# Optimization experiments

Measured on AMD Instinct MI355X. Metric: run time of the kernel, lower is better.

Reference implementation:

```python
import jax, jax.numpy as jnp
import numpy as np


def _fps_one_batch(pts, num_samples):
    """Furthest point sampling for one batch segment.
    pts: [Npb, 3]. Seeds with point 0 (pointops furthestsampling convention).
    Returns int32 indices [num_samples].
    """
    # initial min-distance to the seed point
    dist = jnp.sum((pts - pts[0]) ** 2, axis=-1)  # [Npb]

    def step(dist, _):
        idx = jnp.argmax(dist)                      # furthest remaining point
        d = jnp.sum((pts - pts[idx]) ** 2, axis=-1)  # dist to new sample
        return jnp.minimum(dist, d), idx.astype(jnp.int32)

    _, idxs = jax.lax.scan(step, dist, None, length=num_samples - 1)
    return jnp.concatenate([jnp.zeros((1,), jnp.int32), idxs])


def setup_inputs() -> dict:
    key = jax.random.key(0)
    N, B = 262144, 2
    Npb = N // B
    xyz = jax.random.normal(key, (N, 3), dtype=jnp.float32) * 20.0  # lidar-scale coords
    b = jnp.repeat(jnp.arange(B, dtype=jnp.float32), Npb)[:, None]
    point_bxyz = jnp.concatenate([b, xyz], axis=1)  # [N, 4] (b, x, y, z)
    return {"point_bxyz": point_bxyz, "stride": 32, "batch_size": B}


def reference(point_bxyz, stride, batch_size):
    N = point_bxyz.shape[0]
    Npb = N // batch_size                      # equal-size batch segments
    M = (Npb + stride - 1) // stride           # samples per batch (ceil)
    xyz = point_bxyz[:, 1:4].reshape(batch_size, Npb, 3)

    idx = jax.vmap(lambda p: _fps_one_batch(p, M))(xyz)          # [B, M] local indices
    gidx = idx + (jnp.arange(batch_size, dtype=jnp.int32) * Npb)[:, None]
    new_bxyz = point_bxyz[gidx.reshape(-1)]    # [B*M, 4] sampled points
    return new_bxyz
```

## Files before the change

kernel.cpp:

```cpp
#include <hip/hip_runtime.h>


#define NB    32
#define TPB   256
#define PPT   16
#define NPB   131072
#define MSAMP 4096
#define RING  2
#define KW    8
#define NWAVE 128
#define NQUAD (NWAVE * 16)
#define RB_U32 (NQUAD * 4)
#define NCAND (NWAVE * KW)
#define JCAP  64

typedef unsigned long long u64;
typedef unsigned int u32;
typedef __attribute__((ext_vector_type(4))) u32 u32x4;

__device__ __forceinline__ void st16_sys(u32* p, u32x4 v) {
  asm volatile("global_store_dwordx4 %0, %1, off sc0 sc1"
               :: "v"(p), "v"(v) : "memory");
}
__device__ __forceinline__ void ld16x8_sys(
    const u32* p0, const u32* p1, const u32* p2, const u32* p3,
    const u32* p4, const u32* p5, const u32* p6, const u32* p7,
    u32x4& q0, u32x4& q1, u32x4& q2, u32x4& q3,
    u32x4& q4, u32x4& q5, u32x4& q6, u32x4& q7) {
  asm volatile(
    "global_load_dwordx4 %0, %8, off sc0 sc1\n\t"
    "global_load_dwordx4 %1, %9, off sc0 sc1\n\t"
    "global_load_dwordx4 %2, %10, off sc0 sc1\n\t"
    "global_load_dwordx4 %3, %11, off sc0 sc1\n\t"
    "global_load_dwordx4 %4, %12, off sc0 sc1\n\t"
    "global_load_dwordx4 %5, %13, off sc0 sc1\n\t"
    "global_load_dwordx4 %6, %14, off sc0 sc1\n\t"
    "global_load_dwordx4 %7, %15, off sc0 sc1\n\t"
    "s_waitcnt vmcnt(0)"
    : "=v"(q0), "=v"(q1), "=v"(q2), "=v"(q3),
      "=v"(q4), "=v"(q5), "=v"(q6), "=v"(q7)
    : "v"(p0), "v"(p1), "v"(p2), "v"(p3),
      "v"(p4), "v"(p5), "v"(p6), "v"(p7)
    : "memory");
}

template<int CTRL>
__device__ __forceinline__ u64 dpp_move64(u64 x) {
  int lo = (int)(u32)(x & 0xFFFFFFFFull);
  int hi = (int)(u32)(x >> 32);
  int nlo = __builtin_amdgcn_update_dpp(lo, lo, CTRL, 0xF, 0xF, false);
  int nhi = __builtin_amdgcn_update_dpp(hi, hi, CTRL, 0xF, 0xF, false);
  return ((u64)(u32)nhi << 32) | (u64)(u32)nlo;
}
#define DPP_ROW_SHR(n)  (0x110 + (n))
#define DPP_BCAST15     0x142
#define DPP_BCAST31     0x143

__device__ __forceinline__ u64 dpp_max64_to63(u64 k) {
  u64 t;
  t = dpp_move64<DPP_ROW_SHR(1)>(k); if (t > k) k = t;
  t = dpp_move64<DPP_ROW_SHR(2)>(k); if (t > k) k = t;
  t = dpp_move64<DPP_ROW_SHR(4)>(k); if (t > k) k = t;
  t = dpp_move64<DPP_ROW_SHR(8)>(k); if (t > k) k = t;
  t = dpp_move64<DPP_BCAST15>(k);    if (t > k) k = t;
  t = dpp_move64<DPP_BCAST31>(k);    if (t > k) k = t;
  return k;
}
__device__ __forceinline__ u64 bcast_key(u64 k, int srclane) {
  u32 lo = (u32)__builtin_amdgcn_readlane((int)(u32)(k & 0xFFFFFFFFull), srclane);
  u32 hi = (u32)__builtin_amdgcn_readlane((int)(u32)(k >> 32), srclane);
  return ((u64)hi << 32) | (u64)lo;
}
__device__ __forceinline__ float bcast_f32(float v, int srclane) {
  return __uint_as_float((u32)__builtin_amdgcn_readlane((int)__float_as_uint(v), srclane));
}

struct BMax { u64 k; float x, y, z; };
__device__ __forceinline__ BMax block_max(u64 tk, float tx, float ty, float tz,
    int lane, int wv, int sb,
    u64* s_key, float* s_cx, float* s_cy, float* s_cz) {
  u64 wk = bcast_key(dpp_max64_to63(tk), 63);
  int wl = __ffsll(__ballot(tk == wk)) - 1;
  float wx = bcast_f32(tx, wl), wy = bcast_f32(ty, wl), wz = bcast_f32(tz, wl);
  if (lane == 0) { s_key[sb+wv]=wk; s_cx[sb+wv]=wx; s_cy[sb+wv]=wy; s_cz[sb+wv]=wz; }
  __syncthreads();
  u64 k0=s_key[sb],k1=s_key[sb+1],k2=s_key[sb+2],k3=s_key[sb+3];
  int bi=sb; u64 bk=k0;
  if (k1>bk){bk=k1;bi=sb+1;}
  if (k2>bk){bk=k2;bi=sb+2;}
  if (k3>bk){bk=k3;bi=sb+3;}
  BMax r; r.k=bk; r.x=s_cx[bi]; r.y=s_cy[bi]; r.z=s_cz[bi];
  return r;
}

template<int NC>
__device__ __forceinline__ int sim_wave(const u32* s_pool, int m, u32 cutd,
    int jmax, int lane, float& ox, float& oy, float& oz) {
#pragma clang fp contract(off)
  u64 ck[NC]; float cx[NC], cy[NC], cz[NC];
#pragma unroll
  for (int i = 0; i < NC; ++i) {
    int idx = lane + i * 64;
    if (idx < m) {
      const u32* b = s_pool + idx * 5;
      ck[i] = ((u64)b[1] << 32) | (u64)b[0];
      cx[i] = __uint_as_float(b[2]); cy[i] = __uint_as_float(b[3]);
      cz[i] = __uint_as_float(b[4]);
    } else { ck[i] = 0; cx[i] = cy[i] = cz[i] = 0.f; }
  }
  int j = 0;
  for (int t = 0; t < jmax; ++t) {
    u64 tk = ck[0]; float mx = cx[0], my = cy[0], mz = cz[0];
#pragma unroll
    for (int i = 1; i < NC; ++i)
      if (ck[i] > tk) { tk = ck[i]; mx = cx[i]; my = cy[i]; mz = cz[i]; }
    u64 wk = bcast_key(dpp_max64_to63(tk), 63);
    if (t > 0 && (u32)(wk >> 32) <= cutd) break;
    int wl = __ffsll(__ballot(tk == wk)) - 1;
    float wx = bcast_f32(mx, wl), wy = bcast_f32(my, wl), wz = bcast_f32(mz, wl);
    if (lane == t) { ox = wx; oy = wy; oz = wz; }
    j = t + 1;
#pragma unroll
    for (int i = 0; i < NC; ++i) {
      float dx = cx[i]-wx, dy = cy[i]-wy, dz = cz[i]-wz;
      float d2 = __fadd_rn(__fadd_rn(__fmul_rn(dx,dx), __fmul_rn(dy,dy)),
                           __fmul_rn(dz,dz));
      float nd = fminf(__uint_as_float((u32)(ck[i] >> 32)), d2);
      ck[i] = ((u64)__float_as_uint(nd) << 32) | (ck[i] & 0xFFFFFFFFull);
    }
  }
  return j;
}

__device__ __forceinline__ int sim_block(const u32* s_pool, int m, u32 cutd,
    int jmax, int tid, int lane, int wv, int& sb,
    u64* s_key, float* s_cx, float* s_cy, float* s_cz, float (*s_win)[3]) {
#pragma clang fp contract(off)
  u64 ck[4]; float cx[4], cy[4], cz[4];
#pragma unroll
  for (int i = 0; i < 4; ++i) {
    int idx = tid + i * 256;
    if (idx < m) {
      const u32* b = s_pool + idx * 5;
      ck[i] = ((u64)b[1] << 32) | (u64)b[0];
      cx[i] = __uint_as_float(b[2]); cy[i] = __uint_as_float(b[3]);
      cz[i] = __uint_as_float(b[4]);
    } else { ck[i] = 0; cx[i] = cy[i] = cz[i] = 0.f; }
  }
  int j = 0;
  for (int t = 0; t < jmax; ++t) {
    u64 tk = ck[0]; float mx = cx[0], my = cy[0], mz = cz[0];
#pragma unroll
    for (int i = 1; i < 4; ++i)
      if (ck[i] > tk) { tk = ck[i]; mx = cx[i]; my = cy[i]; mz = cz[i]; }
    BMax w = block_max(tk, mx, my, mz, lane, wv, sb, s_key, s_cx, s_cy, s_cz);
    sb ^= 4;
    if (t > 0 && (u32)(w.k >> 32) <= cutd) break;
    if (tid == 0) { s_win[t][0]=w.x; s_win[t][1]=w.y; s_win[t][2]=w.z; }
    j = t + 1;
#pragma unroll
    for (int i = 0; i < 4; ++i) {
      float dx = cx[i]-w.x, dy = cy[i]-w.y, dz = cz[i]-w.z;
      float d2 = __fadd_rn(__fadd_rn(__fmul_rn(dx,dx), __fmul_rn(dy,dy)),
                           __fmul_rn(dz,dz));
      float nd = fminf(__uint_as_float((u32)(ck[i] >> 32)), d2);
      ck[i] = ((u64)__float_as_uint(nd) << 32) | (ck[i] & 0xFFFFFFFFull);
    }
  }
  __syncthreads();
  return j;
}

__global__ __launch_bounds__(TPB, 1)
void fps_kernel(const float4* __restrict__ pts, float* __restrict__ out,
                u32* __restrict__ slots)
{
#pragma clang fp contract(off)
  const int batch = blockIdx.x >> 5;
  const int rank  = blockIdx.x & (NB - 1);
  const int tid   = threadIdx.x;
  const int lane  = tid & 63;
  const int wv    = tid >> 6;
  const int ws_id = rank * 4 + wv;

  __shared__ u32   s_quads[NWAVE * 68];
  __shared__ u32   s_pool[NCAND * 5];
  __shared__ float s_win[JCAP][3];
  __shared__ u64   s_key[8];
  __shared__ float s_cx[8], s_cy[8], s_cz[8];
  __shared__ int   s_cnt2[2];

  const float4* bpts = pts + (size_t)batch * NPB;
  u32* bslots = slots + (size_t)batch * (RING * RB_U32);
  const int base = rank * (TPB * PPT);

  float px[PPT], py[PPT], pz[PPT], dist[PPT];
  float4 seed = bpts[0];
  const float sx = seed.y, sy = seed.z, sz = seed.w;
#pragma unroll
  for (int k = 0; k < PPT; ++k) {
    float4 p = bpts[base + k * TPB + tid];
    px[k] = p.y; py[k] = p.z; pz[k] = p.w;
    float dx = px[k]-sx, dy = py[k]-sy, dz = pz[k]-sz;
    dist[k] = __fadd_rn(__fadd_rn(__fmul_rn(dx,dx), __fmul_rn(dy,dy)),
                        __fmul_rn(dz,dz));
  }
  if (rank == 0 && tid == 0) {
    float4 o; o.x=(float)batch; o.y=sx; o.z=sy; o.w=sz;
    *(float4*)(out + (size_t)batch * MSAMP * 4) = o;
  }
  if (tid == 0) { s_cnt2[0] = 0; s_cnt2[1] = 0; }
  __syncthreads();

  int S = 0; u32 r = 0; int sb = 0;

  while (S < MSAMP - 1) {
    r += 1;
    const int rem = (MSAMP - 1) - S;
    const int jmax = (rem < JCAP) ? rem : JCAP;

    u32 mask = 0; u64 tk = 0; float tx=0.f, ty=0.f, tz=0.f; int tbk = 0;
#pragma unroll
    for (int k = 0; k < PPT; ++k) {
      u64 kk = ((u64)__float_as_uint(dist[k]) << 32) | ((u64)r << 17) |
               (u64)(0x1FFFF - (base + k * TPB + tid));
      if (kk > tk) { tk = kk; tx = px[k]; ty = py[k]; tz = pz[k]; tbk = k; }
    }
    u32x4 shipq;
    for (int c = 0; c < KW; ++c) {
      u64 wk = bcast_key(dpp_max64_to63(tk), 63);
      int wl = __ffsll(__ballot(tk == wk)) - 1;
      float wx = bcast_f32(tx, wl), wy = bcast_f32(ty, wl), wz = bcast_f32(tz, wl);
      if (lane == 2*c)     { shipq.x=(u32)(wk & 0xFFFFFFFFull); shipq.y=(u32)(wk>>32);
                             shipq.z=__float_as_uint(wx); shipq.w=__float_as_uint(wy); }
      if (lane == 2*c + 1) { shipq.x=r; shipq.y=__float_as_uint(wz);
                             shipq.z=0u; shipq.w=0u; }
      if (tk == wk) {
        mask |= 1u << tbk;
        tk = 0; tx = ty = tz = 0.f; tbk = 0;
#pragma unroll
        for (int k = 0; k < PPT; ++k) {
          if (!((mask >> k) & 1u)) {
            u64 kk = ((u64)__float_as_uint(dist[k]) << 32) | ((u64)r << 17) |
                     (u64)(0x1FFFF - (base + k * TPB + tid));
            if (kk > tk) { tk = kk; tx = px[k]; ty = py[k]; tz = pz[k]; tbk = k; }
          }
        }
      }
    }

    u32* ring = bslots + (size_t)(r & (RING - 1)) * RB_U32;
    if (lane < 16) st16_sys(ring + (ws_id * 16 + lane) * 4, shipq);

    const int gb = wv * 512 + lane;
    const u32 *pp0 = ring + (gb      ) * 4, *pp1 = ring + (gb +  64) * 4,
              *pp2 = ring + (gb + 128) * 4, *pp3 = ring + (gb + 192) * 4,
              *pp4 = ring + (gb + 256) * 4, *pp5 = ring + (gb + 320) * 4,
              *pp6 = ring + (gb + 384) * 4, *pp7 = ring + (gb + 448) * 4;
    u32x4 q0,q1,q2,q3,q4,q5,q6,q7;
    for (u32 it = 0; ; ++it) {
      ld16x8_sys(pp0,pp1,pp2,pp3,pp4,pp5,pp6,pp7, q0,q1,q2,q3,q4,q5,q6,q7);
      bool ok;
      if ((lane & 1) == 0)
        ok = ((q0.x>>17)==r)&&((q1.x>>17)==r)&&((q2.x>>17)==r)&&((q3.x>>17)==r)&&
             ((q4.x>>17)==r)&&((q5.x>>17)==r)&&((q6.x>>17)==r)&&((q7.x>>17)==r);
      else
        ok = (q0.x==r)&&(q1.x==r)&&(q2.x==r)&&(q3.x==r)&&
             (q4.x==r)&&(q5.x==r)&&(q6.x==r)&&(q7.x==r);
      if (__ballot(ok) == ~0ull) break;
      __builtin_amdgcn_s_sleep(1);
    }
    if (tid == 0) s_cnt2[(r + 1) & 1] = 0;
    {
      int g = gb;
      *(u32x4*)&s_quads[(g>>4)*68 + (g&15)*4] = q0; g += 64;
      *(u32x4*)&s_quads[(g>>4)*68 + (g&15)*4] = q1; g += 64;
      *(u32x4*)&s_quads[(g>>4)*68 + (g&15)*4] = q2; g += 64;
      *(u32x4*)&s_quads[(g>>4)*68 + (g&15)*4] = q3; g += 64;
      *(u32x4*)&s_quads[(g>>4)*68 + (g&15)*4] = q4; g += 64;
      *(u32x4*)&s_quads[(g>>4)*68 + (g&15)*4] = q5; g += 64;
      *(u32x4*)&s_quads[(g>>4)*68 + (g&15)*4] = q6; g += 64;
      *(u32x4*)&s_quads[(g>>4)*68 + (g&15)*4] = q7;
    }
    __syncthreads();

    u64 cutk;
    {
      int w0 = lane, w1 = lane + 64;
      u64 k0 = ((u64)s_quads[w0*68 + 57] << 32) | (u64)s_quads[w0*68 + 56];
      u64 k1 = ((u64)s_quads[w1*68 + 57] << 32) | (u64)s_quads[w1*68 + 56];
      u64 ct = (k0 > k1) ? k0 : k1;
      cutk = bcast_key(dpp_max64_to63(ct), 63);
    }
    const u32 cutd = (u32)(cutk >> 32);

    int* cnt = &s_cnt2[r & 1];
#pragma unroll
    for (int i = 0; i < 4; ++i) {
      int cg = tid * 4 + i;
      int qb = (cg >> 3) * 68 + (cg & 7) * 8;
      u32 lo = s_quads[qb], hi = s_quads[qb + 1];
      u64 kk = ((u64)hi << 32) | (u64)lo;
      if (kk > cutk) {
        int pos = atomicAdd(cnt, 1);
        u32* d = &s_pool[pos * 5];
        d[0]=lo; d[1]=hi; d[2]=s_quads[qb+2]; d[3]=s_quads[qb+3]; d[4]=s_quads[qb+5];
      }
    }
    __syncthreads();
    const int m = *cnt;

    float ox = 0.f, oy = 0.f, oz = 0.f;
    int j;
    if      (m <=  64) j = sim_wave<1>(s_pool, m, cutd, jmax, lane, ox, oy, oz);
    else if (m <= 128) j = sim_wave<2>(s_pool, m, cutd, jmax, lane, ox, oy, oz);
    else if (m <= 256) j = sim_wave<4>(s_pool, m, cutd, jmax, lane, ox, oy, oz);
    else if (m <= 512) j = sim_wave<8>(s_pool, m, cutd, jmax, lane, ox, oy, oz);
    else {
      j = sim_block(s_pool, m, cutd, jmax, tid, lane, wv, sb,
                    s_key, s_cx, s_cy, s_cz, s_win);
      if (lane < j) { ox = s_win[lane][0]; oy = s_win[lane][1]; oz = s_win[lane][2]; }
    }

    if (rank == 0 && wv == 0 && lane < j) {
      float4 o; o.x = (float)batch; o.y = ox; o.z = oy; o.w = oz;
      *(float4*)(out + (size_t)(batch * MSAMP + S + 1 + lane) * 4) = o;
    }
    for (int i = 0; i < j; ++i) {
      float wx = bcast_f32(ox, i), wy = bcast_f32(oy, i), wz = bcast_f32(oz, i);
#pragma unroll
      for (int k = 0; k < PPT; ++k) {
        float dx = px[k]-wx, dy = py[k]-wy, dz = pz[k]-wz;
        float d2 = __fadd_rn(__fadd_rn(__fmul_rn(dx,dx), __fmul_rn(dy,dy)),
                             __fmul_rn(dz,dz));
        dist[k] = fminf(dist[k], d2);
      }
    }
    S += j;
  }
}

extern "C" void kernel_launch(void* const* d_in, const int* in_sizes, int n_in,
                              void* d_out, int out_size, void* d_ws, size_t ws_size,
                              hipStream_t stream) {
  const float4* pts = (const float4*)d_in[0];
  float* out = (float*)d_out;
  u32* slots = (u32*)d_ws;

  hipMemsetAsync(d_ws, 0, (size_t)2 * RING * RB_U32 * 4, stream);

  dim3 grid(2 * NB), block(TPB);
  hipLaunchKernelGGL(fps_kernel, grid, block, 0, stream, pts, out, slots);
}
```

Measured before the change: 3.668 ms.

## Ship compact keys, sort local top-16, defer distance update past exchange

```diff
diff --git a/kernel.cpp b/kernel.cpp
--- a/kernel.cpp
+++ b/kernel.cpp
@@ -7,11 +7,10 @@
 #define NPB   131072
 #define MSAMP 4096
 #define RING  2
-#define KW    8
+#define KW    16
 #define NWAVE 128
-#define NQUAD (NWAVE * 16)
-#define RB_U32 (NQUAD * 4)
 #define NCAND (NWAVE * KW)
+#define RBU32 (NCAND * 2)
 #define JCAP  64
 
 typedef unsigned long long u64;
@@ -22,25 +21,17 @@
   asm volatile("global_store_dwordx4 %0, %1, off sc0 sc1"
                :: "v"(p), "v"(v) : "memory");
 }
-__device__ __forceinline__ void ld16x8_sys(
+__device__ __forceinline__ void ld16x4_sys(
     const u32* p0, const u32* p1, const u32* p2, const u32* p3,
-    const u32* p4, const u32* p5, const u32* p6, const u32* p7,
-    u32x4& q0, u32x4& q1, u32x4& q2, u32x4& q3,
-    u32x4& q4, u32x4& q5, u32x4& q6, u32x4& q7) {
+    u32x4& q0, u32x4& q1, u32x4& q2, u32x4& q3) {
   asm volatile(
-    "global_load_dwordx4 %0, %8, off sc0 sc1\n\t"
-    "global_load_dwordx4 %1, %9, off sc0 sc1\n\t"
-    "global_load_dwordx4 %2, %10, off sc0 sc1\n\t"
-    "global_load_dwordx4 %3, %11, off sc0 sc1\n\t"
-    "global_load_dwordx4 %4, %12, off sc0 sc1\n\t"
-    "global_load_dwordx4 %5, %13, off sc0 sc1\n\t"
-    "global_load_dwordx4 %6, %14, off sc0 sc1\n\t"
-    "global_load_dwordx4 %7, %15, off sc0 sc1\n\t"
+    "global_load_dwordx4 %0, %4, off sc0 sc1\n\t"
+    "global_load_dwordx4 %1, %5, off sc0 sc1\n\t"
+    "global_load_dwordx4 %2, %6, off sc0 sc1\n\t"
+    "global_load_dwordx4 %3, %7, off sc0 sc1\n\t"
     "s_waitcnt vmcnt(0)"
-    : "=v"(q0), "=v"(q1), "=v"(q2), "=v"(q3),
-      "=v"(q4), "=v"(q5), "=v"(q6), "=v"(q7)
-    : "v"(p0), "v"(p1), "v"(p2), "v"(p3),
-      "v"(p4), "v"(p5), "v"(p6), "v"(p7)
+    : "=v"(q0), "=v"(q1), "=v"(q2), "=v"(q3)
+    : "v"(p0), "v"(p1), "v"(p2), "v"(p3)
     : "memory");
 }
 
@@ -94,32 +85,24 @@
 }
 
 template<int NC>
-__device__ __forceinline__ int sim_wave(const u32* s_pool, int m, u32 cutd,
-    int jmax, int lane, float& ox, float& oy, float& oz) {
+__device__ __forceinline__ int sim_wave(const u64* s_pool, int m, u64 cutk,
+    int jmax, int lane, const float4* bpts,
+    int pj, float pox, float poy, float poz,
+    float& ox, float& oy, float& oz)
+{
 #pragma clang fp contract(off)
   u64 ck[NC]; float cx[NC], cy[NC], cz[NC];
 #pragma unroll
   for (int i = 0; i < NC; ++i) {
     int idx = lane + i * 64;
-    if (idx < m) {
-      const u32* b = s_pool + idx * 5;
-      ck[i] = ((u64)b[1] << 32) | (u64)b[0];
-      cx[i] = __uint_as_float(b[2]); cy[i] = __uint_as_float(b[3]);
-      cz[i] = __uint_as_float(b[4]);
-    } else { ck[i] = 0; cx[i] = cy[i] = cz[i] = 0.f; }
-  }
-  int j = 0;
-  for (int t = 0; t < jmax; ++t) {
-    u64 tk = ck[0]; float mx = cx[0], my = cy[0], mz = cz[0];
-#pragma unroll
-    for (int i = 1; i < NC; ++i)
-      if (ck[i] > tk) { tk = ck[i]; mx = cx[i]; my = cy[i]; mz = cz[i]; }
-    u64 wk = bcast_key(dpp_max64_to63(tk), 63);
-    if (t > 0 && (u32)(wk >> 32) <= cutd) break;
-    int wl = __ffsll(__ballot(tk == wk)) - 1;
-    float wx = bcast_f32(mx, wl), wy = bcast_f32(my, wl), wz = bcast_f32(mz, wl);
-    if (lane == t) { ox = wx; oy = wy; oz = wz; }
-    j = t + 1;
+    bool v = idx < m;
+    u64 k = v ? s_pool[idx] : 0ull;
+    int gi = v ? (int)(0x1FFFFu - (u32)(k & 0x1FFFFull)) : 0;
+    float4 c = bpts[gi];
+    ck[i] = k; cx[i] = c.y; cy[i] = c.z; cz[i] = c.w;
+  }
+  for (int t = 0; t < pj; ++t) {
+    float wx = bcast_f32(pox, t), wy = bcast_f32(poy, t), wz = bcast_f32(poz, t);
 #pragma unroll
     for (int i = 0; i < NC; ++i) {
       float dx = cx[i]-wx, dy = cy[i]-wy, dz = cz[i]-wz;
@@ -129,37 +112,70 @@
       ck[i] = ((u64)__float_as_uint(nd) << 32) | (ck[i] & 0xFFFFFFFFull);
     }
   }
-  return j;
-}
-
-__device__ __forceinline__ int sim_block(const u32* s_pool, int m, u32 cutd,
-    int jmax, int tid, int lane, int wv, int& sb,
-    u64* s_key, float* s_cx, float* s_cy, float* s_cz, float (*s_win)[3]) {
-#pragma clang fp contract(off)
-  u64 ck[4]; float cx[4], cy[4], cz[4];
-#pragma unroll
-  for (int i = 0; i < 4; ++i) {
-    int idx = tid + i * 256;
-    if (idx < m) {
-      const u32* b = s_pool + idx * 5;
-      ck[i] = ((u64)b[1] << 32) | (u64)b[0];
-      cx[i] = __uint_as_float(b[2]); cy[i] = __uint_as_float(b[3]);
-      cz[i] = __uint_as_float(b[4]);
-    } else { ck[i] = 0; cx[i] = cy[i] = cz[i] = 0.f; }
-  }
   int j = 0;
   for (int t = 0; t < jmax; ++t) {
     u64 tk = ck[0]; float mx = cx[0], my = cy[0], mz = cz[0];
 #pragma unroll
-    for (int i = 1; i < 4; ++i)
+    for (int i = 1; i < NC; ++i)
+      if (ck[i] > tk) { tk = ck[i]; mx = cx[i]; my = cy[i]; mz = cz[i]; }
+    u64 wk = bcast_key(dpp_max64_to63(tk), 63);
+    if (wk <= cutk) break;
+    int wl = __ffsll(__ballot(tk == wk)) - 1;
+    float wx = bcast_f32(mx, wl), wy = bcast_f32(my, wl), wz = bcast_f32(mz, wl);
+    if (lane == t) { ox = wx; oy = wy; oz = wz; }
+    j = t + 1;
+#pragma unroll
+    for (int i = 0; i < NC; ++i) {
+      float dx = cx[i]-wx, dy = cy[i]-wy, dz = cz[i]-wz;
+      float d2 = __fadd_rn(__fadd_rn(__fmul_rn(dx,dx), __fmul_rn(dy,dy)),
+                           __fmul_rn(dz,dz));
+      float nd = fminf(__uint_as_float((u32)(ck[i] >> 32)), d2);
+      ck[i] = ((u64)__float_as_uint(nd) << 32) | (ck[i] & 0xFFFFFFFFull);
+    }
+  }
+  return j;
+}
+
+__device__ __forceinline__ int sim_block(const u64* s_pool, int m, u64 cutk,
+    int jmax, int tid, int lane, int wv, int& sb, const float4* bpts,
+    int pj, float pox, float poy, float poz,
+    u64* s_key, float* s_cx, float* s_cy, float* s_cz, float (*s_win)[3])
+{
+#pragma clang fp contract(off)
+  u64 ck[8]; float cx[8], cy[8], cz[8];
+#pragma unroll
+  for (int i = 0; i < 8; ++i) {
+    int idx = tid + i * 256;
+    bool v = idx < m;
+    u64 k = v ? s_pool[idx] : 0ull;
+    int gi = v ? (int)(0x1FFFFu - (u32)(k & 0x1FFFFull)) : 0;
+    float4 c = bpts[gi];
+    ck[i] = k; cx[i] = c.y; cy[i] = c.z; cz[i] = c.w;
+  }
+  for (int t = 0; t < pj; ++t) {
+    float wx = bcast_f32(pox, t), wy = bcast_f32(poy, t), wz = bcast_f32(poz, t);
+#pragma unroll
+    for (int i = 0; i < 8; ++i) {
+      float dx = cx[i]-wx, dy = cy[i]-wy, dz = cz[i]-wz;
+      float d2 = __fadd_rn(__fadd_rn(__fmul_rn(dx,dx), __fmul_rn(dy,dy)),
+                           __fmul_rn(dz,dz));
+      float nd = fminf(__uint_as_float((u32)(ck[i] >> 32)), d2);
+      ck[i] = ((u64)__float_as_uint(nd) << 32) | (ck[i] & 0xFFFFFFFFull);
+    }
+  }
+  int j = 0;
+  for (int t = 0; t < jmax; ++t) {
+    u64 tk = ck[0]; float mx = cx[0], my = cy[0], mz = cz[0];
+#pragma unroll
+    for (int i = 1; i < 8; ++i)
       if (ck[i] > tk) { tk = ck[i]; mx = cx[i]; my = cy[i]; mz = cz[i]; }
     BMax w = block_max(tk, mx, my, mz, lane, wv, sb, s_key, s_cx, s_cy, s_cz);
     sb ^= 4;
-    if (t > 0 && (u32)(w.k >> 32) <= cutd) break;
+    if (w.k <= cutk) break;
     if (tid == 0) { s_win[t][0]=w.x; s_win[t][1]=w.y; s_win[t][2]=w.z; }
     j = t + 1;
 #pragma unroll
-    for (int i = 0; i < 4; ++i) {
+    for (int i = 0; i < 8; ++i) {
       float dx = cx[i]-w.x, dy = cy[i]-w.y, dz = cz[i]-w.z;
       float d2 = __fadd_rn(__fadd_rn(__fmul_rn(dx,dx), __fmul_rn(dy,dy)),
                            __fmul_rn(dz,dz));
@@ -170,6 +186,8 @@
   __syncthreads();
   return j;
 }
+
+#define CE(a,b) { if (sk[a] < sk[b]) { u64 t_ = sk[a]; sk[a] = sk[b]; sk[b] = t_; } }
 
 __global__ __launch_bounds__(TPB, 1)
 void fps_kernel(const float4* __restrict__ pts, float* __restrict__ out,
@@ -183,15 +201,15 @@
   const int wv    = tid >> 6;
   const int ws_id = rank * 4 + wv;
 
-  __shared__ u32   s_quads[NWAVE * 68];
-  __shared__ u32   s_pool[NCAND * 5];
+  __shared__ u64   s_pool[NCAND];
+  __shared__ u64   s_cutq[4];
   __shared__ float s_win[JCAP][3];
   __shared__ u64   s_key[8];
   __shared__ float s_cx[8], s_cy[8], s_cz[8];
   __shared__ int   s_cnt2[2];
 
   const float4* bpts = pts + (size_t)batch * NPB;
-  u32* bslots = slots + (size_t)batch * (RING * RB_U32);
+  u32* bslots = slots + (size_t)batch * (RING * RBU32);
   const int base = rank * (TPB * PPT);
 
   float px[PPT], py[PPT], pz[PPT], dist[PPT];
@@ -213,121 +231,51 @@
   __syncthreads();
 
   int S = 0; u32 r = 0; int sb = 0;
+  int pj = 0; float pox = 0.f, poy = 0.f, poz = 0.f;
+  float ox = 0.f, oy = 0.f, oz = 0.f;
 
   while (S < MSAMP - 1) {
     r += 1;
     const int rem = (MSAMP - 1) - S;
     const int jmax = (rem < JCAP) ? rem : JCAP;
 
-    u32 mask = 0; u64 tk = 0; float tx=0.f, ty=0.f, tz=0.f; int tbk = 0;
-#pragma unroll
-    for (int k = 0; k < PPT; ++k) {
-      u64 kk = ((u64)__float_as_uint(dist[k]) << 32) | ((u64)r << 17) |
-               (u64)(0x1FFFF - (base + k * TPB + tid));
-      if (kk > tk) { tk = kk; tx = px[k]; ty = py[k]; tz = pz[k]; tbk = k; }
-    }
-    u32x4 shipq;
+    u64 sk[16];
+#pragma unroll
+    for (int k = 0; k < PPT; ++k)
+      sk[k] = ((u64)__float_as_uint(dist[k]) << 32) | ((u64)r << 17) |
+              (u64)(0x1FFFFu - (u32)(base + k * TPB + tid));
+    CE(0,1) CE(2,3) CE(4,5) CE(6,7) CE(8,9) CE(10,11) CE(12,13) CE(14,15)
+    CE(0,2) CE(1,3) CE(4,6) CE(5,7) CE(8,10) CE(9,11) CE(12,14) CE(13,15)
+    CE(1,2) CE(5,6) CE(9,10) CE(13,14)
+    CE(0,4) CE(1,5) CE(2,6) CE(3,7) CE(8,12) CE(9,13) CE(10,14) CE(11,15)
+    CE(2,4) CE(3,5) CE(10,12) CE(11,13)
+    CE(1,2) CE(3,4) CE(5,6) CE(9,10) CE(11,12) CE(13,14)
+    CE(0,8) CE(1,9) CE(2,10) CE(3,11) CE(4,12) CE(5,13) CE(6,14) CE(7,15)
+    CE(4,8) CE(5,9) CE(6,10) CE(7,11)
+    CE(2,4) CE(3,5) CE(6,8) CE(7,9) CE(10,12) CE(11,13)
+    CE(1,2) CE(3,4) CE(5,6) CE(7,8) CE(9,10) CE(11,12) CE(13,14)
+
+    u32x4 shipq; shipq.x = shipq.y = shipq.z = shipq.w = 0u;
+#pragma unroll
     for (int c = 0; c < KW; ++c) {
-      u64 wk = bcast_key(dpp_max64_to63(tk), 63);
-      int wl = __ffsll(__ballot(tk == wk)) - 1;
-      float wx = bcast_f32(tx, wl), wy = bcast_f32(ty, wl), wz = bcast_f32(tz, wl);
-      if (lane == 2*c)     { shipq.x=(u32)(wk & 0xFFFFFFFFull); shipq.y=(u32)(wk>>32);
-                             shipq.z=__float_as_uint(wx); shipq.w=__float_as_uint(wy); }
-      if (lane == 2*c + 1) { shipq.x=r; shipq.y=__float_as_uint(wz);
-                             shipq.z=0u; shipq.w=0u; }
-      if (tk == wk) {
-        mask |= 1u << tbk;
-        tk = 0; tx = ty = tz = 0.f; tbk = 0;
-#pragma unroll
-        for (int k = 0; k < PPT; ++k) {
-          if (!((mask >> k) & 1u)) {
-            u64 kk = ((u64)__float_as_uint(dist[k]) << 32) | ((u64)r << 17) |
-                     (u64)(0x1FFFF - (base + k * TPB + tid));
-            if (kk > tk) { tk = kk; tx = px[k]; ty = py[k]; tz = pz[k]; tbk = k; }
-          }
-        }
+      u64 wk = bcast_key(dpp_max64_to63(sk[0]), 63);
+      if (sk[0] == wk) {
+#pragma unroll
+        for (int i = 0; i < 15; ++i) sk[i] = sk[i+1];
+        sk[15] = 0ull;
       }
-    }
-
-    u32* ring = bslots + (size_t)(r & (RING - 1)) * RB_U32;
-    if (lane < 16) st16_sys(ring + (ws_id * 16 + lane) * 4, shipq);
-
-    const int gb = wv * 512 + lane;
-    const u32 *pp0 = ring + (gb      ) * 4, *pp1 = ring + (gb +  64) * 4,
-              *pp2 = ring + (gb + 128) * 4, *pp3 = ring + (gb + 192) * 4,
-              *pp4 = ring + (gb + 256) * 4, *pp5 = ring + (gb + 320) * 4,
-              *pp6 = ring + (gb + 384) * 4, *pp7 = ring + (gb + 448) * 4;
-    u32x4 q0,q1,q2,q3,q4,q5,q6,q7;
-    for (u32 it = 0; ; ++it) {
-      ld16x8_sys(pp0,pp1,pp2,pp3,pp4,pp5,pp6,pp7, q0,q1,q2,q3,q4,q5,q6,q7);
-      bool ok;
-      if ((lane & 1) == 0)
-        ok = ((q0.x>>17)==r)&&((q1.x>>17)==r)&&((q2.x>>17)==r)&&((q3.x>>17)==r)&&
-             ((q4.x>>17)==r)&&((q5.x>>17)==r)&&((q6.x>>17)==r)&&((q7.x>>17)==r);
-      else
-        ok = (q0.x==r)&&(q1.x==r)&&(q2.x==r)&&(q3.x==r)&&
-             (q4.x==r)&&(q5.x==r)&&(q6.x==r)&&(q7.x==r);
-      if (__ballot(ok) == ~0ull) break;
-      __builtin_amdgcn_s_sleep(1);
-    }
-    if (tid == 0) s_cnt2[(r + 1) & 1] = 0;
-    {
-      int g = gb;
-      *(u32x4*)&s_quads[(g>>4)*68 + (g&15)*4] = q0; g += 64;
-      *(u32x4*)&s_quads[(g>>4)*68 + (g&15)*4] = q1; g += 64;
-      *(u32x4*)&s_quads[(g>>4)*68 + (g&15)*4] = q2; g += 64;
-      *(u32x4*)&s_quads[(g>>4)*68 + (g&15)*4] = q3; g += 64;
-      *(u32x4*)&s_quads[(g>>4)*68 + (g&15)*4] = q4; g += 64;
-      *(u32x4*)&s_quads[(g>>4)*68 + (g&15)*4] = q5; g += 64;
-      *(u32x4*)&s_quads[(g>>4)*68 + (g&15)*4] = q6; g += 64;
-      *(u32x4*)&s_quads[(g>>4)*68 + (g&15)*4] = q7;
-    }
-    __syncthreads();
-
-    u64 cutk;
-    {
-      int w0 = lane, w1 = lane + 64;
-      u64 k0 = ((u64)s_quads[w0*68 + 57] << 32) | (u64)s_quads[w0*68 + 56];
-      u64 k1 = ((u64)s_quads[w1*68 + 57] << 32) | (u64)s_quads[w1*68 + 56];
-      u64 ct = (k0 > k1) ? k0 : k1;
-      cutk = bcast_key(dpp_max64_to63(ct), 63);
-    }
-    const u32 cutd = (u32)(cutk >> 32);
-
-    int* cnt = &s_cnt2[r & 1];
-#pragma unroll
-    for (int i = 0; i < 4; ++i) {
-      int cg = tid * 4 + i;
-      int qb = (cg >> 3) * 68 + (cg & 7) * 8;
-      u32 lo = s_quads[qb], hi = s_quads[qb + 1];
-      u64 kk = ((u64)hi << 32) | (u64)lo;
-      if (kk > cutk) {
-        int pos = atomicAdd(cnt, 1);
-        u32* d = &s_pool[pos * 5];
-        d[0]=lo; d[1]=hi; d[2]=s_quads[qb+2]; d[3]=s_quads[qb+3]; d[4]=s_quads[qb+5];
+      u32 lo = (u32)(wk & 0xFFFFFFFFull), hi = (u32)(wk >> 32);
+      if (lane == (c >> 1)) {
+        if (c & 1) { shipq.z = lo; shipq.w = hi; }
+        else       { shipq.x = lo; shipq.y = hi; }
       }
     }
-    __syncthreads();
-    const int m = *cnt;
-
-    float ox = 0.f, oy = 0.f, oz = 0.f;
-    int j;
-    if      (m <=  64) j = sim_wave<1>(s_pool, m, cutd, jmax, lane, ox, oy, oz);
-    else if (m <= 128) j = sim_wave<2>(s_pool, m, cutd, jmax, lane, ox, oy, oz);
-    else if (m <= 256) j = sim_wave<4>(s_pool, m, cutd, jmax, lane, ox, oy, oz);
-    else if (m <= 512) j = sim_wave<8>(s_pool, m, cutd, jmax, lane, ox, oy, oz);
-    else {
-      j = sim_block(s_pool, m, cutd, jmax, tid, lane, wv, sb,
-                    s_key, s_cx, s_cy, s_cz, s_win);
-      if (lane < j) { ox = s_win[lane][0]; oy = s_win[lane][1]; oz = s_win[lane][2]; }
-    }
-
-    if (rank == 0 && wv == 0 && lane < j) {
-      float4 o; o.x = (float)batch; o.y = ox; o.z = oy; o.w = oz;
-      *(float4*)(out + (size_t)(batch * MSAMP + S + 1 + lane) * 4) = o;
-    }
-    for (int i = 0; i < j; ++i) {
-      float wx = bcast_f32(ox, i), wy = bcast_f32(oy, i), wz = bcast_f32(oz, i);
+
+    u32* ring = bslots + (size_t)(r & 1u) * RBU32;
+    if (lane < 8) st16_sys(ring + (ws_id * 16 + lane * 2) * 2, shipq);
+
+    for (int t = 0; t < pj; ++t) {
+      float wx = bcast_f32(pox, t), wy = bcast_f32(poy, t), wz = bcast_f32(poz, t);
 #pragma unroll
       for (int k = 0; k < PPT; ++k) {
         float dx = px[k]-wx, dy = py[k]-wy, dz = pz[k]-wz;
@@ -336,7 +284,77 @@
         dist[k] = fminf(dist[k], d2);
       }
     }
-    S += j;
+
+    const int cb = wv * 512 + lane * 2;
+    const u32 *P0 = ring + (cb      ) * 2, *P1 = ring + (cb + 128) * 2,
+              *P2 = ring + (cb + 256) * 2, *P3 = ring + (cb + 384) * 2;
+    u32x4 q0, q1, q2, q3;
+    for (;;) {
+      ld16x4_sys(P0, P1, P2, P3, q0, q1, q2, q3);
+      bool ok = ((q0.x>>17)==r) && ((q0.z>>17)==r) && ((q1.x>>17)==r) &&
+                ((q1.z>>17)==r) && ((q2.x>>17)==r) && ((q2.z>>17)==r) &&
+                ((q3.x>>17)==r) && ((q3.z>>17)==r);
+      if (__ballot(ok) == ~0ull) break;
+      __builtin_amdgcn_s_sleep(1);
+    }
+
+    u64 cm = 0ull;
+    if ((lane & 7) == 7) {
+      u64 a0 = ((u64)q0.w << 32) | (u64)q0.z;
+      u64 a1 = ((u64)q1.w << 32) | (u64)q1.z;
+      u64 a2 = ((u64)q2.w << 32) | (u64)q2.z;
+      u64 a3 = ((u64)q3.w << 32) | (u64)q3.z;
+      cm = a0; if (a1 > cm) cm = a1; if (a2 > cm) cm = a2; if (a3 > cm) cm = a3;
+    }
+    u64 qc = bcast_key(dpp_max64_to63(cm), 63);
+    if (lane == 0) s_cutq[wv] = qc;
+    __syncthreads();
+    u64 cutk = s_cutq[0];
+    if (s_cutq[1] > cutk) cutk = s_cutq[1];
+    if (s_cutq[2] > cutk) cutk = s_cutq[2];
+    if (s_cutq[3] > cutk) cutk = s_cutq[3];
+    if (tid == 0) s_cnt2[(r + 1) & 1] = 0;
+
+    u64 kk[8] = { ((u64)q0.y<<32)|q0.x, ((u64)q0.w<<32)|q0.z,
+                  ((u64)q1.y<<32)|q1.x, ((u64)q1.w<<32)|q1.z,
+                  ((u64)q2.y<<32)|q2.x, ((u64)q2.w<<32)|q2.z,
+                  ((u64)q3.y<<32)|q3.x, ((u64)q3.w<<32)|q3.z };
+    bool hh[8]; int myoff[8]; int tot = 0;
+    const u64 ltmask = (lane == 63) ? ~0ull >> 1 : ((1ull << lane) - 1ull);
+#pragma unroll
+    for (int i = 0; i < 8; ++i) {
+      hh[i] = kk[i] > cutk;
+      u64 b = __ballot(hh[i]);
+      myoff[i] = tot + __popcll(b & ltmask);
+      tot += __popcll(b);
+    }
+    int pbase = 0;
+    if (lane == 0) pbase = atomicAdd(&s_cnt2[r & 1], tot);
+    pbase = __builtin_amdgcn_readfirstlane(pbase);
+#pragma unroll
+    for (int i = 0; i < 8; ++i)
+      if (hh[i]) s_pool[pbase + myoff[i]] = kk[i];
+    __syncthreads();
+    const int m = s_cnt2[r & 1];
+
+    int j;
+    if (m <= 256)
+      j = sim_wave<4>(s_pool, m, cutk, jmax, lane, bpts, pj, pox, poy, poz, ox, oy, oz);
+    else if (m <= 512)
+      j = sim_wave<8>(s_pool, m, cutk, jmax, lane, bpts, pj, pox, poy, poz, ox, oy, oz);
+    else if (m <= 1024)
+      j = sim_wave<16>(s_pool, m, cutk, jmax, lane, bpts, pj, pox, poy, poz, ox, oy, oz);
+    else {
+      j = sim_block(s_pool, m, cutk, jmax, tid, lane, wv, sb, bpts,
+                    pj, pox, poy, poz, s_key, s_cx, s_cy, s_cz, s_win);
+      if (lane < j) { ox = s_win[lane][0]; oy = s_win[lane][1]; oz = s_win[lane][2]; }
+    }
+
+    if (rank == 0 && wv == 0 && lane < j) {
+      float4 o; o.x = (float)batch; o.y = ox; o.z = oy; o.w = oz;
+      *(float4*)(out + (size_t)(batch * MSAMP + S + 1 + lane) * 4) = o;
+    }
+    S += j; pj = j; pox = ox; poy = oy; poz = oz;
   }
 }
 
@@ -347,7 +365,7 @@
   float* out = (float*)d_out;
   u32* slots = (u32*)d_ws;
 
-  hipMemsetAsync(d_ws, 0, (size_t)2 * RING * RB_U32 * 4, stream);
+  hipMemsetAsync(d_ws, 0, (size_t)2 * RING * RBU32 * 4, stream);
 
   dim3 grid(2 * NB), block(TPB);
   hipLaunchKernelGGL(fps_kernel, grid, block, 0, stream, pts, out, slots);
```

New measurement: 5.396 ms. 47.1% more time.
